# Performance work log

Measured on AMD Instinct MI355X. Metric: run time of the kernel, lower is better.

## Reference

```python
import jax, jax.numpy as jnp
import numpy as np
from jax import lax

EPS = 1e-08


def setup_inputs() -> dict:
    key = jax.random.key(0)
    k1, k2, k3 = jax.random.split(key, 3)
    B, I, O, H, W_, K = 16, 512, 512, 32, 32, 3
    x = jax.random.normal(k1, (B, I, H, W_), dtype=jnp.float32)
    s = jax.random.uniform(k2, (B, I), dtype=jnp.float32)
    weight = jax.random.normal(k3, (O, I, K, K), dtype=jnp.float32)
    return {"x": x, "s": s, "weight": weight}


def reference(x, s, weight):
    # x: [B, I, H, W], s: [B, I], weight: [O, I, kH, kW]
    B, I, H, Wd = x.shape
    O = weight.shape[0]
    # Per-sample modulated weights: [B, O, I, kH, kW]
    # (faithful to source: the weight_scale multiply is dead code, overwritten)
    Wm = s[:, None, :, None, None] * weight[None]
    # Demodulation: L2-normalize each per-sample output filter
    sigma = jnp.sqrt(jnp.sum(Wm * Wm, axis=(2, 3, 4), keepdims=True) + EPS)
    Wm = Wm / sigma
    # Grouped conv with groups = batch_size (same trick as torch source)
    x_g = x.reshape(1, B * I, H, Wd)
    W_g = Wm.reshape(B * O, I, *weight.shape[-2:])
    out = lax.conv_general_dilated(
        x_g, W_g,
        window_strides=(1, 1),
        padding='SAME',
        feature_group_count=B,
        dimension_numbers=('NCHW', 'OIHW', 'NCHW'),
    )
    return out.reshape(B, O, out.shape[-2], out.shape[-1])
```

## Files before the change

kernel.cpp:

```cpp
#include <hip/hip_runtime.h>
#include <hip/hip_bf16.h>
#include <stdint.h>

#define BATCH 16
#define CIN   512
#define COUT  512
#define HH    32
#define WW    32
#define HP    34
#define HWN   1024
#define EPS_  1e-8f

#define NTILES 72
#define BUFBYTES 32768
#define LDS_BYTES (2*BUFBYTES)

typedef __attribute__((ext_vector_type(8))) short bf16x8;
typedef __attribute__((ext_vector_type(4))) float f32x4;
typedef __attribute__((address_space(1))) void gvoid;
typedef __attribute__((address_space(3))) void lvoid;

#define XS_OFF    0
#define XS_BYTES  (BATCH*HP*HP*CIN*2)
#define WT_OFF    (XS_OFF + XS_BYTES)
#define WT_BYTES  (9*COUT*CIN*2)
#define ISG_OFF   (WT_OFF + WT_BYTES)

__global__ __launch_bounds__(256)
void prep_all(const float* __restrict__ x, const float* __restrict__ s,
              const float* __restrict__ w,
              __hip_bfloat16* __restrict__ xs, __hip_bfloat16* __restrict__ wt,
              float* __restrict__ isg) {
  __shared__ __align__(16) char smem[35328];
  const int bid = blockIdx.x;
  const int tid = threadIdx.x;

  if (bid < BATCH * 34) {
    unsigned short (*tile)[520] = (unsigned short (*)[520])smem;
    float* ssh = (float*)(smem + 33280);
    const int hp = bid % 34;
    const int b  = bid / 34;
    __hip_bfloat16* rowbase = xs + (((size_t)(b * HP + hp)) * HP) * CIN;

    if (hp == 0 || hp == 33) {
      for (int j = tid; j < HP * CIN / 8; j += 256)
        ((int4*)rowbase)[j] = make_int4(0, 0, 0, 0);
      return;
    }
    if (tid < 64)        ((int4*)rowbase)[tid] = make_int4(0, 0, 0, 0);
    else if (tid < 128)  ((int4*)(rowbase + 33 * CIN))[tid - 64] = make_int4(0, 0, 0, 0);

    ssh[tid]       = s[b * CIN + tid];
    ssh[256 + tid] = s[b * CIN + 256 + tid];
    __syncthreads();

    const int h = hp - 1;
    const int r = tid >> 3;
    const int c = tid & 7;
    const float* xbase = x + (size_t)b * CIN * HWN + h * WW;
#pragma unroll
    for (int p = 0; p < 16; ++p) {
      int i = p * 32 + r;
      float4 v = *(const float4*)(xbase + (size_t)i * HWN + c * 4);
      float sc = ssh[i];
#pragma unroll
      for (int j = 0; j < 4; ++j) {
        float f = ((const float*)&v)[j] * sc;
        __hip_bfloat16 hb = __float2bfloat16(f);
        tile[c * 4 + j][i] = *(unsigned short*)&hb;
      }
    }
    __syncthreads();

    const int wq = tid >> 3;
    const int i0 = (tid & 7) * 64;
    __hip_bfloat16* dst = rowbase + (wq + 1) * CIN + i0;
    const int4* src = (const int4*)&tile[wq][i0];
#pragma unroll
    for (int q = 0; q < 8; ++q)
      ((int4*)dst)[q] = src[q];
  } else {
    const int o = bid - BATCH * 34;
    float* wrow = (float*)smem;
    {
      const float4* wsrc = (const float4*)(w + (size_t)o * CIN * 9);
      float4* wdst = (float4*)wrow;
      for (int j = tid; j < CIN * 9 / 4; j += 256)
        wdst[j] = wsrc[j];
    }
    __syncthreads();

    float ss[2];
#pragma unroll
    for (int u = 0; u < 2; ++u) {
      int i = tid + u * 256;
      float acc = 0.f;
#pragma unroll
      for (int k = 0; k < 9; ++k) {
        float v = wrow[i * 9 + k];
        acc += v * v;
        wt[(size_t)k * COUT * CIN + o * CIN + i] = __float2bfloat16(v);
      }
      ss[u] = acc;
    }
    __syncthreads();

    float* s2 = (float*)smem;
    float (*red)[4] = (float (*)[4])(smem + 32768);
    for (int j = tid; j < BATCH * CIN; j += 256) {
      float v = s[j];
      s2[j] = v * v;
    }
    __syncthreads();

    float accb[16];
#pragma unroll
    for (int b = 0; b < 16; ++b) accb[b] = 0.f;
#pragma unroll
    for (int u = 0; u < 2; ++u) {
      int i = tid + u * 256;
      float q = ss[u];
#pragma unroll
      for (int b = 0; b < 16; ++b) accb[b] += q * s2[b * CIN + i];
    }
#pragma unroll
    for (int b = 0; b < 16; ++b) {
#pragma unroll
      for (int off = 32; off; off >>= 1) accb[b] += __shfl_xor(accb[b], off);
      if ((tid & 63) == 0) red[b][tid >> 6] = accb[b];
    }
    __syncthreads();
    if (tid < 16) {
      float tot = red[tid][0] + red[tid][1] + red[tid][2] + red[tid][3];
      isg[tid * COUT + o] = 1.0f / sqrtf(tot + EPS_);
    }
  }
}

__global__ __launch_bounds__(256, 2)
void conv_db(const __hip_bfloat16* __restrict__ xs,
             const __hip_bfloat16* __restrict__ wt,
             const float* __restrict__ isg,
             float* __restrict__ out) {
  extern __shared__ __align__(16) char lds[];

  const int bid = blockIdx.x;
  const int nt = bid & 7;
  const int mt = (bid >> 3) & 3;
  const int b  = bid >> 5;
  const int m0  = mt * 128;
  const int hw0 = nt * 128;

  const int t  = threadIdx.x;
  const int wv = t >> 6;
  const int l  = t & 63;
  const int wr = wv >> 1;
  const int wc = wv & 1;
  const int segbase = wv * 4;

  int baseA[4], baseB[4];
#pragma unroll
  for (int q = 0; q < 4; ++q) {
    int seg = segbase + q;
    int r = seg * 8 + (l >> 3);
    int swz = (l & 7) ^ (l >> 3);
    baseA[q] = (m0 + r) * CIN + swz * 8;
    int n_abs = hw0 + r;
    int hB = n_abs >> 5, wB = n_abs & 31;
    baseB[q] = ((b * HP + hB) * HP + wB) * CIN + swz * 8;
  }

  int offA[2][4], offB[2][4];
#pragma unroll
  for (int kk = 0; kk < 2; ++kk) {
#pragma unroll
    for (int f = 0; f < 4; ++f) {
      int slot = ((kk * 4) + (l >> 4)) ^ (l & 7);
      offA[kk][f] = (wr * 64 + f * 16 + (l & 15)) * 128 + slot * 16;
      offB[kk][f] = (wc * 64 + f * 16 + (l & 15)) * 128 + slot * 16;
    }
  }

  f32x4 acc[4][4];
#pragma unroll
  for (int m = 0; m < 4; ++m)
#pragma unroll
    for (int n = 0; n < 4; ++n)
      acc[m][n] = (f32x4){0.f, 0.f, 0.f, 0.f};

#define TILE_OFFS(tt, gA, gB)                                   \
  {                                                             \
    int tap = (tt) >> 3, ic = (tt) & 7;                         \
    int kh = (tap * 11) >> 5;                                   \
    int kw = tap - kh * 3;                                      \
    gA = tap * (COUT * CIN) + ic * 64;                          \
    gB = (kh * HP + kw) * CIN + ic * 64;                        \
  }

#define STAGE(tt, buf)                                                      \
  {                                                                         \
    int gA_, gB_;                                                           \
    TILE_OFFS(tt, gA_, gB_);                                                \
    char* dA_ = lds + (buf) * BUFBYTES;                                     \
    char* dB_ = dA_ + 16384;                                                \
    _Pragma("unroll")                                                       \
    for (int q = 0; q < 4; ++q)                                             \
      __builtin_amdgcn_global_load_lds(                                     \
          (gvoid*)(const void*)(wt + gA_ + baseA[q]),                       \
          (lvoid*)(dA_ + (segbase + q) * 1024), 16, 0, 0);                  \
    _Pragma("unroll")                                                       \
    for (int q = 0; q < 4; ++q)                                             \
      __builtin_amdgcn_global_load_lds(                                     \
          (gvoid*)(const void*)(xs + gB_ + baseB[q]),                       \
          (lvoid*)(dB_ + (segbase + q) * 1024), 16, 0, 0);                  \
  }

  STAGE(0, 0);
  __syncthreads();

  int buf = 0;
#pragma unroll 1
  for (int tt = 0; tt < NTILES; ++tt) {
    if (tt + 1 < NTILES) STAGE(tt + 1, buf ^ 1);
    const char* pA = lds + buf * BUFBYTES;
    const char* pB = pA + 16384;
#pragma unroll
    for (int kk = 0; kk < 2; ++kk) {
      bf16x8 af[4], bfr[4];
#pragma unroll
      for (int f = 0; f < 4; ++f) af[f]  = *(const bf16x8*)(pA + offA[kk][f]);
#pragma unroll
      for (int f = 0; f < 4; ++f) bfr[f] = *(const bf16x8*)(pB + offB[kk][f]);
#pragma unroll
      for (int m = 0; m < 4; ++m)
#pragma unroll
        for (int n = 0; n < 4; ++n)
          acc[m][n] = __builtin_amdgcn_mfma_f32_16x16x32_bf16(
              af[m], bfr[n], acc[m][n], 0, 0, 0);
    }
    __syncthreads();
    buf ^= 1;
  }

#pragma unroll
  for (int m = 0; m < 4; ++m) {
#pragma unroll
    for (int j = 0; j < 4; ++j) {
      int o = m0 + wr * 64 + m * 16 + (l >> 4) * 4 + j;
      float sg = isg[b * COUT + o];
      float* orow = out + ((size_t)(b * COUT + o)) * HWN + hw0 + wc * 64 + (l & 15);
#pragma unroll
      for (int n = 0; n < 4; ++n)
        orow[n * 16] = acc[m][n][j] * sg;
    }
  }
}

extern "C" void kernel_launch(void* const* d_in, const int* in_sizes, int n_in,
                              void* d_out, int out_size, void* d_ws, size_t ws_size,
                              hipStream_t stream) {
  const float* x = (const float*)d_in[0];
  const float* s = (const float*)d_in[1];
  const float* w = (const float*)d_in[2];
  float* out = (float*)d_out;
  char* ws = (char*)d_ws;
  __hip_bfloat16* xs  = (__hip_bfloat16*)(ws + XS_OFF);
  __hip_bfloat16* wt  = (__hip_bfloat16*)(ws + WT_OFF);
  float*          isg = (float*)(ws + ISG_OFF);

  (void)hipFuncSetAttribute((const void*)conv_db,
                            hipFuncAttributeMaxDynamicSharedMemorySize, LDS_BYTES);

  hipLaunchKernelGGL(prep_all, dim3(BATCH * 34 + COUT), dim3(256), 0, stream,
                     x, s, w, xs, wt, isg);
  hipLaunchKernelGGL(conv_db, dim3(512), dim3(256), LDS_BYTES, stream,
                     xs, wt, isg, out);
}
```

Measured before the change: 167.0 us.

## Deepen conv pipeline with split A/B staging, vmcnt waits and MFMA priority

The conv kernel replaces its double-buffered combined A+B stage with separate LDS rings: two slots for weights and three for activations, with activation tiles prefetched two iterations ahead. Full __syncthreads drains are replaced by s_waitcnt vmcnt(4) plus a raw barrier, and s_setprio raises wave priority around the MFMA block. The aim is to keep global-to-LDS loads in flight across iterations and hide memory latency. The prep kernel also reads weights straight from global instead of via LDS and drops one barrier. LDS use grows to 80KB per block, which with two blocks per CU may approach the LDS limit, and the hand-counted waitcnt values are fragile.

```diff
diff --git a/kernel.cpp b/kernel.cpp
--- a/kernel.cpp
+++ b/kernel.cpp
@@ -12,8 +12,8 @@
 #define EPS_  1e-8f
 
 #define NTILES 72
-#define BUFBYTES 32768
-#define LDS_BYTES (2*BUFBYTES)
+#define SLOT   16384
+#define LDS_BYTES (5*SLOT)
 
 typedef __attribute__((ext_vector_type(8))) short bf16x8;
 typedef __attribute__((ext_vector_type(4))) float f32x4;
@@ -80,39 +80,28 @@
     for (int q = 0; q < 8; ++q)
       ((int4*)dst)[q] = src[q];
   } else {
+    float* s2  = (float*)smem;
+    float (*red)[4] = (float (*)[4])(smem + 32768);
     const int o = bid - BATCH * 34;
-    float* wrow = (float*)smem;
-    {
-      const float4* wsrc = (const float4*)(w + (size_t)o * CIN * 9);
-      float4* wdst = (float4*)wrow;
-      for (int j = tid; j < CIN * 9 / 4; j += 256)
-        wdst[j] = wsrc[j];
-    }
-    __syncthreads();
-
+    for (int j = tid; j < BATCH * CIN; j += 256) {
+      float v = s[j];
+      s2[j] = v * v;
+    }
     float ss[2];
 #pragma unroll
     for (int u = 0; u < 2; ++u) {
       int i = tid + u * 256;
+      const float* wp = w + ((size_t)o * CIN + i) * 9;
       float acc = 0.f;
 #pragma unroll
       for (int k = 0; k < 9; ++k) {
-        float v = wrow[i * 9 + k];
+        float v = wp[k];
         acc += v * v;
         wt[(size_t)k * COUT * CIN + o * CIN + i] = __float2bfloat16(v);
       }
       ss[u] = acc;
     }
     __syncthreads();
-
-    float* s2 = (float*)smem;
-    float (*red)[4] = (float (*)[4])(smem + 32768);
-    for (int j = tid; j < BATCH * CIN; j += 256) {
-      float v = s[j];
-      s2[j] = v * v;
-    }
-    __syncthreads();
-
     float accb[16];
 #pragma unroll
     for (int b = 0; b < 16; ++b) accb[b] = 0.f;
@@ -138,11 +127,13 @@
 }
 
 __global__ __launch_bounds__(256, 2)
-void conv_db(const __hip_bfloat16* __restrict__ xs,
-             const __hip_bfloat16* __restrict__ wt,
-             const float* __restrict__ isg,
-             float* __restrict__ out) {
+void conv_cnt(const __hip_bfloat16* __restrict__ xs,
+              const __hip_bfloat16* __restrict__ wt,
+              const float* __restrict__ isg,
+              float* __restrict__ out) {
   extern __shared__ __align__(16) char lds[];
+  char* ldsA = lds;
+  char* ldsB = lds + 2 * SLOT;
 
   const int bid = blockIdx.x;
   const int nt = bid & 7;
@@ -188,26 +179,27 @@
     for (int n = 0; n < 4; ++n)
       acc[m][n] = (f32x4){0.f, 0.f, 0.f, 0.f};
 
-#define TILE_OFFS(tt, gA, gB)                                   \
-  {                                                             \
-    int tap = (tt) >> 3, ic = (tt) & 7;                         \
-    int kh = (tap * 11) >> 5;                                   \
-    int kw = tap - kh * 3;                                      \
-    gA = tap * (COUT * CIN) + ic * 64;                          \
-    gB = (kh * HP + kw) * CIN + ic * 64;                        \
-  }
-
-#define STAGE(tt, buf)                                                      \
+#define STAGE_A(tt, sl)                                                     \
   {                                                                         \
-    int gA_, gB_;                                                           \
-    TILE_OFFS(tt, gA_, gB_);                                                \
-    char* dA_ = lds + (buf) * BUFBYTES;                                     \
-    char* dB_ = dA_ + 16384;                                                \
+    int tc_ = (tt) < NTILES ? (tt) : NTILES - 1;                            \
+    int tap_ = tc_ >> 3, ic_ = tc_ & 7;                                     \
+    int gA_ = tap_ * (COUT * CIN) + ic_ * 64;                               \
+    char* dA_ = ldsA + (sl) * SLOT;                                         \
     _Pragma("unroll")                                                       \
     for (int q = 0; q < 4; ++q)                                             \
       __builtin_amdgcn_global_load_lds(                                     \
           (gvoid*)(const void*)(wt + gA_ + baseA[q]),                       \
           (lvoid*)(dA_ + (segbase + q) * 1024), 16, 0, 0);                  \
+  }
+
+#define STAGE_B(tt, sl)                                                     \
+  {                                                                         \
+    int tc_ = (tt) < NTILES ? (tt) : NTILES - 1;                            \
+    int tap_ = tc_ >> 3, ic_ = tc_ & 7;                                     \
+    int kh_ = (tap_ * 11) >> 5;                                             \
+    int kw_ = tap_ - kh_ * 3;                                               \
+    int gB_ = (kh_ * HP + kw_) * CIN + ic_ * 64;                            \
+    char* dB_ = ldsB + (sl) * SLOT;                                         \
     _Pragma("unroll")                                                       \
     for (int q = 0; q < 4; ++q)                                             \
       __builtin_amdgcn_global_load_lds(                                     \
@@ -215,32 +207,50 @@
           (lvoid*)(dB_ + (segbase + q) * 1024), 16, 0, 0);                  \
   }
 
-  STAGE(0, 0);
-  __syncthreads();
-
-  int buf = 0;
+#define KK_PHASE(kk, pA, pB)                                                \
+  {                                                                         \
+    bf16x8 af[4], bfr[4];                                                   \
+    _Pragma("unroll")                                                       \
+    for (int f = 0; f < 4; ++f) af[f]  = *(const bf16x8*)((pA) + offA[kk][f]); \
+    _Pragma("unroll")                                                       \
+    for (int f = 0; f < 4; ++f) bfr[f] = *(const bf16x8*)((pB) + offB[kk][f]); \
+    __builtin_amdgcn_s_setprio(1);                                          \
+    _Pragma("unroll")                                                       \
+    for (int m = 0; m < 4; ++m)                                             \
+      _Pragma("unroll")                                                     \
+      for (int n = 0; n < 4; ++n)                                           \
+        acc[m][n] = __builtin_amdgcn_mfma_f32_16x16x32_bf16(                \
+            af[m], bfr[n], acc[m][n], 0, 0, 0);                             \
+    __builtin_amdgcn_s_setprio(0);                                          \
+  }
+
+  STAGE_B(0, 0);
+  STAGE_A(0, 0);
+  STAGE_B(1, 1);
+  asm volatile("s_waitcnt vmcnt(4)" ::: "memory");
+  __builtin_amdgcn_sched_barrier(0);
+  __builtin_amdgcn_s_barrier();
+  __builtin_amdgcn_sched_barrier(0);
+
+  int bB = 0;
+  int sB2 = 2;
 #pragma unroll 1
   for (int tt = 0; tt < NTILES; ++tt) {
-    if (tt + 1 < NTILES) STAGE(tt + 1, buf ^ 1);
-    const char* pA = lds + buf * BUFBYTES;
-    const char* pB = pA + 16384;
-#pragma unroll
-    for (int kk = 0; kk < 2; ++kk) {
-      bf16x8 af[4], bfr[4];
-#pragma unroll
-      for (int f = 0; f < 4; ++f) af[f]  = *(const bf16x8*)(pA + offA[kk][f]);
-#pragma unroll
-      for (int f = 0; f < 4; ++f) bfr[f] = *(const bf16x8*)(pB + offB[kk][f]);
-#pragma unroll
-      for (int m = 0; m < 4; ++m)
-#pragma unroll
-        for (int n = 0; n < 4; ++n)
-          acc[m][n] = __builtin_amdgcn_mfma_f32_16x16x32_bf16(
-              af[m], bfr[n], acc[m][n], 0, 0, 0);
-    }
-    __syncthreads();
-    buf ^= 1;
-  }
+    STAGE_A(tt + 1, (tt + 1) & 1);
+    const char* pA = ldsA + (tt & 1) * SLOT;
+    const char* pB = ldsB + bB * SLOT;
+    KK_PHASE(0, pA, pB);
+    STAGE_B(tt + 2, sB2);
+    KK_PHASE(1, pA, pB);
+    asm volatile("s_waitcnt lgkmcnt(0)" ::: "memory");
+    asm volatile("s_waitcnt vmcnt(4)" ::: "memory");
+    __builtin_amdgcn_sched_barrier(0);
+    __builtin_amdgcn_s_barrier();
+    __builtin_amdgcn_sched_barrier(0);
+    bB  = (bB  == 2) ? 0 : bB + 1;
+    sB2 = (sB2 == 2) ? 0 : sB2 + 1;
+  }
+  asm volatile("s_waitcnt vmcnt(0)" ::: "memory");
 
 #pragma unroll
   for (int m = 0; m < 4; ++m) {
@@ -268,11 +278,11 @@
   __hip_bfloat16* wt  = (__hip_bfloat16*)(ws + WT_OFF);
   float*          isg = (float*)(ws + ISG_OFF);
 
-  (void)hipFuncSetAttribute((const void*)conv_db,
+  (void)hipFuncSetAttribute((const void*)conv_cnt,
                             hipFuncAttributeMaxDynamicSharedMemorySize, LDS_BYTES);
 
   hipLaunchKernelGGL(prep_all, dim3(BATCH * 34 + COUT), dim3(256), 0, stream,
                      x, s, w, xs, wt, isg);
-  hipLaunchKernelGGL(conv_db, dim3(512), dim3(256), LDS_BYTES, stream,
+  hipLaunchKernelGGL(conv_cnt, dim3(512), dim3(256), LDS_BYTES, stream,
                      xs, wt, isg, out);
 }
```

After: 164.3 us. About the same (-1.6%).
